# Kernel tuning notes

Measured on AMD Instinct MI355X. Metric: run time of the kernel, lower is better.

## Reference

```python
import jax, jax.numpy as jnp
import numpy as np

B, S, D = 4, 4096, 1024

def setup_inputs() -> dict:
    key = jax.random.key(0)
    ks = jax.random.split(key, 7)
    s = 1.0 / np.sqrt(D)
    return {
        "x": jax.random.normal(ks[0], (B, S, D), dtype=jnp.float32),
        "Wq": jax.random.uniform(ks[1], (D, D), jnp.float32, -s, s),
        "bq": jax.random.uniform(ks[2], (D,), jnp.float32, -s, s),
        "Wk": jax.random.uniform(ks[3], (D, D), jnp.float32, -s, s),
        "bk": jax.random.uniform(ks[4], (D,), jnp.float32, -s, s),
        "Wv": jax.random.uniform(ks[5], (D, D), jnp.float32, -s, s),
        "bv": jax.random.uniform(ks[6], (D,), jnp.float32, -s, s),
    }

def reference(x, Wq, bq, Wk, bk, Wv, bv):
    # q/k/v projections: [B,S,D]
    q = jnp.einsum("bsd,ed->bse", x, Wq) + bq
    k = jnp.einsum("bsd,ed->bse", x, Wk) + bk
    v = jnp.einsum("bsd,ed->bse", x, Wv) + bv
    scale = jnp.asarray(x.shape[-1] ** 0.5, x.dtype)
    scores = jnp.einsum("bqd,bkd->bqk", q, k) / scale  # [B,S,S]
    probs = jax.nn.softmax(scores, axis=-1)
    return jnp.einsum("bqk,bkd->bqd", probs, v)
```

## Files before the change

### kernel.cpp

```cpp
#include <hip/hip_runtime.h>


typedef unsigned short u16;
typedef __attribute__((ext_vector_type(8))) short bf16x8;
typedef __attribute__((ext_vector_type(4))) float f32x4;

__device__ __forceinline__ float bf2f(u16 h) {
    unsigned int x = ((unsigned int)h) << 16;
    float f;
    __builtin_memcpy(&f, &x, 4);
    return f;
}

__device__ __forceinline__ u16 f2bf(float f) {
    unsigned int x;
    __builtin_memcpy(&x, &f, 4);
    unsigned int r = (x + 0x7FFFu + ((x >> 16) & 1u)) >> 16;
    return (u16)r;
}

__device__ __forceinline__ void load16_lds(const u16* g, u16* l) {
    __builtin_amdgcn_global_load_lds(
        (const __attribute__((address_space(1))) void*)g,
        (__attribute__((address_space(3))) void*)l, 16, 0, 0);
}

__global__ __launch_bounds__(256) void cvt_all(
    const float* __restrict__ x, const float* __restrict__ wq,
    const float* __restrict__ wk, const float* __restrict__ wv,
    u16* __restrict__ xo, u16* __restrict__ qo, u16* __restrict__ ko,
    u16* __restrict__ vo, float* __restrict__ L) {
    int i = blockIdx.x * 256 + threadIdx.x;
    if (i >= 4980736) {
        ((float4*)L)[i - 4980736] = (float4){0.f, 0.f, 0.f, 0.f};
        return;
    }
    const float* src;
    u16* dst;
    int idx;
    if (i < 4194304) {
        src = x; dst = xo; idx = i;
    } else {
        int j = i - 4194304;
        int sel = j >> 18;
        idx = j & 262143;
        src = (sel == 0) ? wq : (sel == 1) ? wk : wv;
        dst = (sel == 0) ? qo : (sel == 1) ? ko : vo;
    }
    float4 f = ((const float4*)src)[idx];
    ushort4 o;
    o.x = f2bf(f.x); o.y = f2bf(f.y); o.z = f2bf(f.z); o.w = f2bf(f.w);
    ((ushort4*)dst)[idx] = o;
}

__device__ __forceinline__ void mfma_core(
    const u16* __restrict__ A, const u16* __restrict__ B, int K, int ldA,
    int ldB, size_t rowA0, size_t rowB0, u16* As, u16* Bs, f32x4 acc[4][4]) {
    const int t = threadIdx.x;
    const int lane = t & 63;
    const int wave = t >> 6;
    const int wm = (wave >> 1) * 64;
    const int wn = (wave & 1) * 64;
    const int lm = lane & 15;
    const int qd = lane >> 4;
    const int kx = lm & 7;
    const int rl = lane >> 3;
    const int swz = ((lane & 7) ^ rl) << 3;

#pragma unroll
    for (int i = 0; i < 4; ++i)
#pragma unroll
        for (int j = 0; j < 4; ++j) acc[i][j] = (f32x4){0.f, 0.f, 0.f, 0.f};

    const u16* ga = A + (rowA0 + (size_t)(wave * 32 + rl)) * (size_t)ldA + swz;
    const u16* gb = B + (rowB0 + (size_t)(wave * 32 + rl)) * (size_t)ldB + swz;
    u16* la = As + wave * 2048;
    u16* lb = Bs + wave * 2048;

    for (int kb = 0; kb < K; kb += 64) {
#pragma unroll
        for (int p = 0; p < 4; ++p) {
            load16_lds(ga + (size_t)(p * 8) * ldA + kb, la + p * 512);
            load16_lds(gb + (size_t)(p * 8) * ldB + kb, lb + p * 512);
        }
        __syncthreads();
#pragma unroll
        for (int k0 = 0; k0 < 64; k0 += 32) {
            const int q0 = k0 >> 3;
            const int cofs = (((q0 + qd) ^ kx) << 3);
            bf16x8 a[4], b[4];
#pragma unroll
            for (int i = 0; i < 4; ++i) {
                a[i] = *(const bf16x8*)(As + (wm + i * 16 + lm) * 64 + cofs);
                b[i] = *(const bf16x8*)(Bs + (wn + i * 16 + lm) * 64 + cofs);
            }
#pragma unroll
            for (int i = 0; i < 4; ++i)
#pragma unroll
                for (int j = 0; j < 4; ++j)
                    acc[i][j] = __builtin_amdgcn_mfma_f32_16x16x32_bf16(
                        a[i], b[j], acc[i][j], 0, 0, 0);
        }
        __syncthreads();
    }
}

__global__ __launch_bounds__(256, 4) void proj_qkv(
    const u16* __restrict__ x, const u16* __restrict__ w0,
    const u16* __restrict__ w1, const u16* __restrict__ w2,
    const float* __restrict__ b0, const float* __restrict__ b1,
    const float* __restrict__ b2, u16* __restrict__ Qb, u16* __restrict__ Kb,
    u16* __restrict__ Vt) {
    __shared__ __align__(16) u16 As[128 * 64];
    __shared__ __align__(16) u16 Bs[128 * 64];
    const int z = blockIdx.z;
    const u16* W = (z == 0) ? w0 : (z == 1) ? w1 : w2;
    const float* bias = (z == 0) ? b0 : (z == 1) ? b1 : b2;

    const size_t rowA0 = (size_t)blockIdx.y * 128;
    const size_t rowB0 = (size_t)blockIdx.x * 128;
    f32x4 acc[4][4];
    mfma_core(x, W, 1024, 1024, 1024, rowA0, rowB0, As, Bs, acc);

    const int lane = threadIdx.x & 63;
    const int wave = threadIdx.x >> 6;
    const int wm = (wave >> 1) * 64;
    const int wn = (wave & 1) * 64;
    const int lm = lane & 15;
    const int qd = lane >> 4;

#pragma unroll
    for (int i = 0; i < 4; ++i) {
        const int r0 = (int)rowA0 + wm + i * 16 + qd * 4;
#pragma unroll
        for (int j = 0; j < 4; ++j) {
            const int col = (int)rowB0 + wn + j * 16 + lm;
            const float bv = bias[col];
            if (z < 2) {
                u16* C = z ? Kb : Qb;
#pragma unroll
                for (int r = 0; r < 4; ++r)
                    C[(size_t)(r0 + r) * 1024 + col] = f2bf(acc[i][j][r] + bv);
            } else {
                const int batch = r0 >> 12;
                const int s0 = r0 & 4095;
                ushort4 o;
                o.x = f2bf(acc[i][j][0] + bv);
                o.y = f2bf(acc[i][j][1] + bv);
                o.z = f2bf(acc[i][j][2] + bv);
                o.w = f2bf(acc[i][j][3] + bv);
                *(ushort4*)(Vt + (size_t)batch * 4194304 +
                            (size_t)col * 4096 + s0) = o;
            }
        }
    }
}

__global__ __launch_bounds__(256, 4) void gemm_scores(
    const u16* __restrict__ Qb, const u16* __restrict__ Kb,
    u16* __restrict__ SP, float* __restrict__ L) {
    __shared__ __align__(16) u16 As[128 * 64];
    __shared__ __align__(16) u16 Bs[128 * 64];
    __shared__ float Ls[256];
    const size_t z = blockIdx.z;
    const u16* A = Qb + z * 4194304;
    const u16* B = Kb + z * 4194304;
    u16* C = SP + z * 16777216;

    const size_t rowA0 = (size_t)blockIdx.x * 128;
    const size_t rowB0 = (size_t)blockIdx.y * 128;
    f32x4 acc[4][4];
    mfma_core(A, B, 1024, 1024, 1024, rowA0, rowB0, As, Bs, acc);

    const int lane = threadIdx.x & 63;
    const int wave = threadIdx.x >> 6;
    const int wm = (wave >> 1) * 64;
    const int wn = (wave & 1) * 64;
    const int lm = lane & 15;
    const int qd = lane >> 4;

#pragma unroll
    for (int i = 0; i < 4; ++i) {
        const int rl0 = wm + i * 16 + qd * 4;
        float part[4] = {0.f, 0.f, 0.f, 0.f};
#pragma unroll
        for (int j = 0; j < 4; ++j) {
            const int col = (int)rowB0 + wn + j * 16 + lm;
            u16 o[4];
#pragma unroll
            for (int r = 0; r < 4; ++r) {
                float e = __expf(acc[i][j][r] * 0.03125f);
                o[r] = f2bf(e);
                part[r] += e;
            }
#pragma unroll
            for (int r = 0; r < 4; ++r)
                C[(size_t)(rowA0 + rl0 + r) * 4096 + col] = o[r];
        }
#pragma unroll
        for (int r = 0; r < 4; ++r) {
#pragma unroll
            for (int o = 8; o >= 1; o >>= 1) part[r] += __shfl_xor(part[r], o);
        }
        if (lm == 0) {
#pragma unroll
            for (int r = 0; r < 4; ++r)
                Ls[(rl0 + r) * 2 + (wave & 1)] = part[r];
        }
    }
    __syncthreads();
    const int t = threadIdx.x;
    if (t < 128)
        atomicAdd(L + z * 4096 + rowA0 + t, Ls[t * 2] + Ls[t * 2 + 1]);
}

__global__ __launch_bounds__(256, 4) void gemm_pv(
    const u16* __restrict__ SP, const u16* __restrict__ Vt,
    float* __restrict__ out, const float* __restrict__ L) {
    __shared__ __align__(16) u16 As[128 * 64];
    __shared__ __align__(16) u16 Bs[128 * 64];
    const size_t z = blockIdx.z;
    const u16* A = SP + z * 16777216;
    const u16* B = Vt + z * 4194304;
    float* C = out + z * 4194304;

    const size_t rowA0 = (size_t)blockIdx.x * 128;
    const size_t rowB0 = (size_t)blockIdx.y * 128;
    f32x4 acc[4][4];
    mfma_core(A, B, 4096, 4096, 4096, rowA0, rowB0, As, Bs, acc);

    float* Lsh = (float*)As;
    const int t = threadIdx.x;
    if (t < 128) Lsh[t] = 1.0f / L[z * 4096 + rowA0 + t];
    __syncthreads();

    const int lane = t & 63;
    const int wave = t >> 6;
    const int wm = (wave >> 1) * 64;
    const int wn = (wave & 1) * 64;
    const int lm = lane & 15;
    const int qd = lane >> 4;

#pragma unroll
    for (int i = 0; i < 4; ++i) {
        const int rl0 = wm + i * 16 + qd * 4;
        const int r0 = (int)rowA0 + rl0;
#pragma unroll
        for (int j = 0; j < 4; ++j) {
            const int col = (int)rowB0 + wn + j * 16 + lm;
#pragma unroll
            for (int r = 0; r < 4; ++r)
                C[(size_t)(r0 + r) * 1024 + col] = acc[i][j][r] * Lsh[rl0 + r];
        }
    }
}

template <int MODE>
__global__ __launch_bounds__(256, 3) void gemm_nt(
    const u16* __restrict__ A, const u16* __restrict__ B,
    void* __restrict__ Cv, int K, int ldA, int ldB, int ldC, float scale) {
    __shared__ __align__(16) u16 As[128 * 64];
    __shared__ __align__(16) u16 Bs[128 * 64];
    const size_t rowA0 = (size_t)blockIdx.y * 128;
    const size_t rowB0 = (size_t)blockIdx.x * 128;
    f32x4 acc[4][4];
    mfma_core(A, B, K, ldA, ldB, rowA0, rowB0, As, Bs, acc);

    const int lane = threadIdx.x & 63;
    const int wave = threadIdx.x >> 6;
    const int wm = (wave >> 1) * 64;
    const int wn = (wave & 1) * 64;
    const int lm = lane & 15;
    const int qd = lane >> 4;

#pragma unroll
    for (int i = 0; i < 4; ++i) {
        const int r0 = (int)rowA0 + wm + i * 16 + qd * 4;
#pragma unroll
        for (int j = 0; j < 4; ++j) {
            const int col = (int)rowB0 + wn + j * 16 + lm;
            if (MODE == 2) {
                u16* C = (u16*)Cv;
#pragma unroll
                for (int r = 0; r < 4; ++r)
                    C[(size_t)(r0 + r) * ldC + col] = f2bf(acc[i][j][r] * scale);
            } else {
                float* C = (float*)Cv;
#pragma unroll
                for (int r = 0; r < 4; ++r)
                    C[(size_t)(r0 + r) * ldC + col] = acc[i][j][r];
            }
        }
    }
}

__global__ __launch_bounds__(256) void softmax_inplace(u16* __restrict__ P) {
    u16* p = P + (size_t)blockIdx.x * 4096;
    const int t = threadIdx.x;
    const int lane = t & 63;
    const int wave = t >> 6;
    __shared__ float redmax[4];
    __shared__ float redsum[4];

    uint4 raw0 = *(const uint4*)(p + t * 8);
    uint4 raw1 = *(const uint4*)(p + 2048 + t * 8);
    float v[16];
    {
        const u16* h0 = (const u16*)&raw0;
        const u16* h1 = (const u16*)&raw1;
#pragma unroll
        for (int i = 0; i < 8; ++i) v[i] = bf2f(h0[i]);
#pragma unroll
        for (int i = 0; i < 8; ++i) v[8 + i] = bf2f(h1[i]);
    }
    float m = v[0];
#pragma unroll
    for (int i = 1; i < 16; ++i) m = fmaxf(m, v[i]);
#pragma unroll
    for (int o = 32; o >= 1; o >>= 1) m = fmaxf(m, __shfl_xor(m, o));
    if (lane == 0) redmax[wave] = m;
    __syncthreads();
    m = fmaxf(fmaxf(redmax[0], redmax[1]), fmaxf(redmax[2], redmax[3]));

    float s = 0.f;
#pragma unroll
    for (int i = 0; i < 16; ++i) {
        v[i] = __expf(v[i] - m);
        s += v[i];
    }
#pragma unroll
    for (int o = 32; o >= 1; o >>= 1) s += __shfl_xor(s, o);
    if (lane == 0) redsum[wave] = s;
    __syncthreads();
    s = redsum[0] + redsum[1] + redsum[2] + redsum[3];
    const float inv = 1.0f / s;

    u16 ho[16];
#pragma unroll
    for (int i = 0; i < 16; ++i) ho[i] = f2bf(v[i] * inv);
    *(uint4*)(p + t * 8) = *(const uint4*)&ho[0];
    *(uint4*)(p + 2048 + t * 8) = *(const uint4*)&ho[8];
}

extern "C" void kernel_launch(void* const* d_in, const int* in_sizes, int n_in,
                              void* d_out, int out_size, void* d_ws, size_t ws_size,
                              hipStream_t stream) {
    const float* x  = (const float*)d_in[0];
    const float* Wq = (const float*)d_in[1];
    const float* bq = (const float*)d_in[2];
    const float* Wk = (const float*)d_in[3];
    const float* bk = (const float*)d_in[4];
    const float* Wv = (const float*)d_in[5];
    const float* bv = (const float*)d_in[6];
    float* out = (float*)d_out;

    const bool big = ws_size >= (size_t)234946560;
    char* w = (char*)d_ws;
    u16 *x_bf, *wq_bf, *wk_bf, *wv_bf, *Qb, *Kb, *Vt, *SP;
    float* L = nullptr;
    if (big) {
        SP    = (u16*)(w);
        x_bf  = (u16*)(w);
        wq_bf = (u16*)(w + 33554432);
        wk_bf = (u16*)(w + 35651584);
        wv_bf = (u16*)(w + 37748736);
        Qb    = (u16*)(w + 134217728);
        Kb    = (u16*)(w + 167772160);
        Vt    = (u16*)(w + 201326592);
        L     = (float*)(w + 234881024);
    } else {
        x_bf  = (u16*)(w);
        wq_bf = (u16*)(w + 33554432);
        wk_bf = (u16*)(w + 35651584);
        wv_bf = (u16*)(w + 37748736);
        Qb    = (u16*)(w + 39845888);
        Kb    = (u16*)(w + 73400320);
        Vt    = (u16*)(w + 106954752);
        SP    = (u16*)(w + 140509184);
    }

    cvt_all<<<big ? 19472 : 19456, 256, 0, stream>>>(
        x, Wq, Wk, Wv, x_bf, wq_bf, wk_bf, wv_bf, L);

    proj_qkv<<<dim3(8, 128, 3), 256, 0, stream>>>(
        x_bf, wq_bf, wk_bf, wv_bf, bq, bk, bv, Qb, Kb, Vt);

    if (big) {
        gemm_scores<<<dim3(32, 32, 4), 256, 0, stream>>>(Qb, Kb, SP, L);
        gemm_pv<<<dim3(32, 8, 4), 256, 0, stream>>>(SP, Vt, out, L);
    } else {
        for (int b = 0; b < 4; ++b) {
            const size_t off = (size_t)b * 4194304;
            gemm_nt<2><<<dim3(32, 32, 1), 256, 0, stream>>>(
                Qb + off, Kb + off, SP, 1024, 1024, 1024, 4096, 0.03125f);
            softmax_inplace<<<4096, 256, 0, stream>>>(SP);
            gemm_nt<3><<<dim3(8, 32, 1), 256, 0, stream>>>(
                SP, Vt + off, out + off, 4096, 4096, 4096, 1024, 1.f);
        }
    }
}
```

Measured before the change: 534.0 us.

## Replace scores GEMM with 256x256-tile, 8-wave, double-buffered pipelined kernel

The QK^T scores kernel now uses 256x256 output tiles with 512 threads and 128KB of dynamic LDS. It double-buffers K-slices through direct global-to-LDS loads with swizzled addressing. Explicit waitcnt, barriers and setprio interleave the MFMA phases with the next-stage loads. This is meant to raise data reuse per tile and hide load latency. In exchange it reduces occupancy and adds a large per-thread accumulator footprint, which raises register pressure.

After: 539.2 us. No clear change (+1.0%).

```diff
diff --git a/kernel.cpp b/kernel.cpp
--- a/kernel.cpp
+++ b/kernel.cpp
@@ -156,40 +156,156 @@
     }
 }
 
-__global__ __launch_bounds__(256, 4) void gemm_scores(
+__global__ __launch_bounds__(512, 2) void gemm_scores256(
     const u16* __restrict__ Qb, const u16* __restrict__ Kb,
     u16* __restrict__ SP, float* __restrict__ L) {
-    __shared__ __align__(16) u16 As[128 * 64];
-    __shared__ __align__(16) u16 Bs[128 * 64];
-    __shared__ float Ls[256];
+    extern __shared__ __align__(16) u16 sm[];
     const size_t z = blockIdx.z;
     const u16* A = Qb + z * 4194304;
     const u16* B = Kb + z * 4194304;
     u16* C = SP + z * 16777216;
-
-    const size_t rowA0 = (size_t)blockIdx.x * 128;
-    const size_t rowB0 = (size_t)blockIdx.y * 128;
-    f32x4 acc[4][4];
-    mfma_core(A, B, 1024, 1024, 1024, rowA0, rowB0, As, Bs, acc);
-
-    const int lane = threadIdx.x & 63;
-    const int wave = threadIdx.x >> 6;
-    const int wm = (wave >> 1) * 64;
-    const int wn = (wave & 1) * 64;
-    const int lm = lane & 15;
-    const int qd = lane >> 4;
-
-#pragma unroll
-    for (int i = 0; i < 4; ++i) {
-        const int rl0 = wm + i * 16 + qd * 4;
+    const int rowA0 = blockIdx.x * 256;
+    const int rowB0 = blockIdx.y * 256;
+
+    const int t = threadIdx.x;
+    const int l = t & 63;
+    const int w = t >> 6;
+    const int wr = w >> 2;
+    const int wc = w & 3;
+    const int lm = l & 15;
+    const int qd = l >> 4;
+    const int rsw = (lm >> 1) & 3;
+    const int srow = l >> 2;
+    const int csw = (l & 3) ^ ((l >> 3) & 3);
+    const int roff = (qd ^ rsw) * 8;
+
+    f32x4 acc[8][4];
+#pragma unroll
+    for (int i = 0; i < 8; ++i)
+#pragma unroll
+        for (int j = 0; j < 4; ++j) acc[i][j] = (f32x4){0.f, 0.f, 0.f, 0.f};
+
+    auto STAGE = [&](int M, int s, int ks, int bs) {
+        const u16* G = M ? B : A;
+        const int r0 = M ? rowB0 : rowA0;
+        u16* lb = sm + M * 32768 + bs * 16384 + ks * 8192 + w * 512;
+        const u16* g = G + (size_t)(r0 + w * 16 + srow) * 1024 +
+                       (s * 64 + ks * 32 + csw * 8);
+        load16_lds(g, lb);
+        load16_lds(g + (size_t)128 * 1024, lb + 4096);
+    };
+
+    STAGE(0, 0, 0, 0); STAGE(1, 0, 0, 0);
+    STAGE(0, 0, 1, 0); STAGE(1, 0, 1, 0);
+    STAGE(0, 1, 0, 1); STAGE(1, 1, 0, 1);
+    asm volatile("s_waitcnt vmcnt(8)" ::: "memory");
+    asm volatile("s_barrier" ::: "memory");
+    __builtin_amdgcn_sched_barrier(0);
+
+    const int NS = 16;
+#pragma unroll 2
+    for (int s = 0; s < NS; ++s) {
+        const int cur = s & 1;
+        const u16* As_ = sm + cur * 16384;
+        const u16* Bs_ = sm + 32768 + cur * 16384;
+        bf16x8 a[4], b[4];
+
+#pragma unroll
+        for (int m = 0; m < 4; ++m)
+            a[m] = *(const bf16x8*)(As_ + (wr * 128 + m * 16 + lm) * 32 + roff);
+#pragma unroll
+        for (int n = 0; n < 4; ++n)
+            b[n] = *(const bf16x8*)(Bs_ + (wc * 64 + n * 16 + lm) * 32 + roff);
+        if (s + 1 < NS) STAGE(0, s + 1, 1, (s + 1) & 1);
+        asm volatile("s_barrier" ::: "memory");
+        __builtin_amdgcn_sched_barrier(0);
+        __builtin_amdgcn_s_setprio(1);
+#pragma unroll
+        for (int m = 0; m < 4; ++m)
+#pragma unroll
+            for (int n = 0; n < 4; ++n)
+                acc[m][n] = __builtin_amdgcn_mfma_f32_16x16x32_bf16(
+                    a[m], b[n], acc[m][n], 0, 0, 0);
+        __builtin_amdgcn_s_setprio(0);
+        __builtin_amdgcn_sched_barrier(0);
+        asm volatile("s_barrier" ::: "memory");
+        __builtin_amdgcn_sched_barrier(0);
+
+#pragma unroll
+        for (int m = 0; m < 4; ++m)
+            a[m] = *(const bf16x8*)(As_ + (wr * 128 + 64 + m * 16 + lm) * 32 + roff);
+        if (s + 1 < NS) STAGE(1, s + 1, 1, (s + 1) & 1);
+        if (s < NS - 1) asm volatile("s_waitcnt vmcnt(8)" ::: "memory");
+        else            asm volatile("s_waitcnt vmcnt(0)" ::: "memory");
+        asm volatile("s_barrier" ::: "memory");
+        __builtin_amdgcn_sched_barrier(0);
+        __builtin_amdgcn_s_setprio(1);
+#pragma unroll
+        for (int m = 0; m < 4; ++m)
+#pragma unroll
+            for (int n = 0; n < 4; ++n)
+                acc[4 + m][n] = __builtin_amdgcn_mfma_f32_16x16x32_bf16(
+                    a[m], b[n], acc[4 + m][n], 0, 0, 0);
+        __builtin_amdgcn_s_setprio(0);
+        __builtin_amdgcn_sched_barrier(0);
+        asm volatile("s_barrier" ::: "memory");
+        __builtin_amdgcn_sched_barrier(0);
+
+#pragma unroll
+        for (int m = 0; m < 4; ++m)
+            a[m] = *(const bf16x8*)(As_ + 8192 + (wr * 128 + m * 16 + lm) * 32 + roff);
+#pragma unroll
+        for (int n = 0; n < 4; ++n)
+            b[n] = *(const bf16x8*)(Bs_ + 8192 + (wc * 64 + n * 16 + lm) * 32 + roff);
+        if (s + 2 < NS) STAGE(0, s + 2, 0, s & 1);
+        asm volatile("s_barrier" ::: "memory");
+        __builtin_amdgcn_sched_barrier(0);
+        __builtin_amdgcn_s_setprio(1);
+#pragma unroll
+        for (int m = 0; m < 4; ++m)
+#pragma unroll
+            for (int n = 0; n < 4; ++n)
+                acc[m][n] = __builtin_amdgcn_mfma_f32_16x16x32_bf16(
+                    a[m], b[n], acc[m][n], 0, 0, 0);
+        __builtin_amdgcn_s_setprio(0);
+        __builtin_amdgcn_sched_barrier(0);
+        asm volatile("s_barrier" ::: "memory");
+        __builtin_amdgcn_sched_barrier(0);
+
+#pragma unroll
+        for (int m = 0; m < 4; ++m)
+            a[m] = *(const bf16x8*)(As_ + 8192 + (wr * 128 + 64 + m * 16 + lm) * 32 + roff);
+        if (s + 2 < NS) STAGE(1, s + 2, 0, s & 1);
+        if (s < NS - 2)       asm volatile("s_waitcnt vmcnt(8)" ::: "memory");
+        else if (s == NS - 2) asm volatile("s_waitcnt vmcnt(4)" ::: "memory");
+        else                  asm volatile("s_waitcnt vmcnt(0)" ::: "memory");
+        asm volatile("s_barrier" ::: "memory");
+        __builtin_amdgcn_sched_barrier(0);
+        __builtin_amdgcn_s_setprio(1);
+#pragma unroll
+        for (int m = 0; m < 4; ++m)
+#pragma unroll
+            for (int n = 0; n < 4; ++n)
+                acc[4 + m][n] = __builtin_amdgcn_mfma_f32_16x16x32_bf16(
+                    a[m], b[n], acc[4 + m][n], 0, 0, 0);
+        __builtin_amdgcn_s_setprio(0);
+        __builtin_amdgcn_sched_barrier(0);
+        asm volatile("s_barrier" ::: "memory");
+        __builtin_amdgcn_sched_barrier(0);
+    }
+
+    float* Ls = (float*)sm;
+#pragma unroll
+    for (int i = 0; i < 8; ++i) {
+        const int rl0 = wr * 128 + i * 16 + qd * 4;
         float part[4] = {0.f, 0.f, 0.f, 0.f};
 #pragma unroll
-        for (int j = 0; j < 4; ++j) {
-            const int col = (int)rowB0 + wn + j * 16 + lm;
+        for (int n = 0; n < 4; ++n) {
+            const int col = rowB0 + wc * 64 + n * 16 + lm;
             u16 o[4];
 #pragma unroll
             for (int r = 0; r < 4; ++r) {
-                float e = __expf(acc[i][j][r] * 0.03125f);
+                float e = __expf(acc[i][n][r] * 0.03125f);
                 o[r] = f2bf(e);
                 part[r] += e;
             }
@@ -204,14 +320,13 @@
         }
         if (lm == 0) {
 #pragma unroll
-            for (int r = 0; r < 4; ++r)
-                Ls[(rl0 + r) * 2 + (wave & 1)] = part[r];
+            for (int r = 0; r < 4; ++r) Ls[(rl0 + r) * 4 + wc] = part[r];
         }
     }
     __syncthreads();
-    const int t = threadIdx.x;
-    if (t < 128)
-        atomicAdd(L + z * 4096 + rowA0 + t, Ls[t * 2] + Ls[t * 2 + 1]);
+    if (t < 256)
+        atomicAdd(L + z * 4096 + rowA0 + t,
+                  Ls[t * 4] + Ls[t * 4 + 1] + Ls[t * 4 + 2] + Ls[t * 4 + 3]);
 }
 
 __global__ __launch_bounds__(256, 4) void gemm_pv(
@@ -353,6 +468,13 @@
     const float* Wv = (const float*)d_in[5];
     const float* bv = (const float*)d_in[6];
     float* out = (float*)d_out;
+
+    static bool attr_done = false;
+    if (!attr_done) {
+        hipFuncSetAttribute(reinterpret_cast<const void*>(gemm_scores256),
+                            hipFuncAttributeMaxDynamicSharedMemorySize, 131072);
+        attr_done = true;
+    }
 
     const bool big = ws_size >= (size_t)234946560;
     char* w = (char*)d_ws;
@@ -386,7 +508,7 @@
         x_bf, wq_bf, wk_bf, wv_bf, bq, bk, bv, Qb, Kb, Vt);
 
     if (big) {
-        gemm_scores<<<dim3(32, 32, 4), 256, 0, stream>>>(Qb, Kb, SP, L);
+        gemm_scores256<<<dim3(16, 16, 4), 512, 131072, stream>>>(Qb, Kb, SP, L);
         gemm_pv<<<dim3(32, 8, 4), 256, 0, stream>>>(SP, Vt, out, L);
     } else {
         for (int b = 0; b < 4; ++b) {
```

## Enlarge scores GEMM tile to 256x256 with triple-buffered LDS pipeline

Applied to the files above, without the earlier changes.

Replaces the 128x128 scores kernel with a 256x256-tile, 512-thread kernel that stages Q and K slices via direct global-to-LDS loads into a three-stage ring buffer and uses swizzled LDS addressing. Each wave computes a 128x64 subtile, which raises operand reuse and halves the number of blocks reading Q/K. The softmax-numerator exp and row-sum epilogue is kept, now reducing across four column waves. It needs 96KB of dynamic shared memory and more accumulator registers, which lowers occupancy.

Result: slower. 547.0 us (+2.4%).

```diff
diff --git a/kernel.cpp b/kernel.cpp
--- a/kernel.cpp
+++ b/kernel.cpp
@@ -156,40 +156,89 @@
     }
 }
 
-__global__ __launch_bounds__(256, 4) void gemm_scores(
+__global__ __launch_bounds__(512, 2) void gemm_scores256(
     const u16* __restrict__ Qb, const u16* __restrict__ Kb,
     u16* __restrict__ SP, float* __restrict__ L) {
-    __shared__ __align__(16) u16 As[128 * 64];
-    __shared__ __align__(16) u16 Bs[128 * 64];
-    __shared__ float Ls[256];
+    extern __shared__ __align__(16) u16 sm[];
     const size_t z = blockIdx.z;
-    const u16* A = Qb + z * 4194304;
-    const u16* B = Kb + z * 4194304;
+    const u16* Ag = Qb + z * 4194304;
+    const u16* Bg = Kb + z * 4194304;
     u16* C = SP + z * 16777216;
-
-    const size_t rowA0 = (size_t)blockIdx.x * 128;
-    const size_t rowB0 = (size_t)blockIdx.y * 128;
-    f32x4 acc[4][4];
-    mfma_core(A, B, 1024, 1024, 1024, rowA0, rowB0, As, Bs, acc);
-
-    const int lane = threadIdx.x & 63;
-    const int wave = threadIdx.x >> 6;
-    const int wm = (wave >> 1) * 64;
-    const int wn = (wave & 1) * 64;
-    const int lm = lane & 15;
-    const int qd = lane >> 4;
-
-#pragma unroll
-    for (int i = 0; i < 4; ++i) {
-        const int rl0 = wm + i * 16 + qd * 4;
+    const int rowA0 = blockIdx.x * 256;
+    const int rowB0 = blockIdx.y * 256;
+
+    const int t = threadIdx.x;
+    const int l = t & 63;
+    const int w = t >> 6;
+    const int wr = w >> 2;
+    const int wc = w & 3;
+    const int lm = l & 15;
+    const int qd = l >> 4;
+    const int roff = (qd ^ ((lm >> 1) & 3)) * 8;
+    const int csw = (l & 3) ^ ((l >> 3) & 3);
+
+    f32x4 acc[8][4];
+#pragma unroll
+    for (int i = 0; i < 8; ++i)
+#pragma unroll
+        for (int j = 0; j < 4; ++j) acc[i][j] = (f32x4){0.f, 0.f, 0.f, 0.f};
+
+    auto STAGE = [&](int M, int s, int bs) {
+        const u16* G = M ? Bg : Ag;
+        const int r0 = M ? rowB0 : rowA0;
+        u16* lb = sm + M * 24576 + bs * 8192 + w * 512;
+        const u16* g = G + (size_t)(r0 + w * 16 + (l >> 2)) * 1024 +
+                       (s * 32 + csw * 8);
+        load16_lds(g, lb);
+        load16_lds(g + (size_t)128 * 1024, lb + 4096);
+    };
+
+    STAGE(0, 0, 0); STAGE(1, 0, 0);
+    STAGE(0, 1, 1); STAGE(1, 1, 1);
+    asm volatile("s_waitcnt vmcnt(4)" ::: "memory");
+    asm volatile("s_barrier" ::: "memory");
+
+    const int NS = 32;
+    for (int s = 0; s < NS; ++s) {
+        const int cur = s % 3;
+        if (s + 2 < NS) {
+            const int stg = (s + 2) % 3;
+            STAGE(0, s + 2, stg);
+            STAGE(1, s + 2, stg);
+        }
+        const u16* Ab = sm + cur * 8192;
+        const u16* Bb = sm + 24576 + cur * 8192;
+        bf16x8 a[8], b[4];
+#pragma unroll
+        for (int m = 0; m < 8; ++m)
+            a[m] = *(const bf16x8*)(Ab + (wr * 128 + m * 16 + lm) * 32 + roff);
+#pragma unroll
+        for (int n = 0; n < 4; ++n)
+            b[n] = *(const bf16x8*)(Bb + (wc * 64 + n * 16 + lm) * 32 + roff);
+#pragma unroll
+        for (int m = 0; m < 8; ++m)
+#pragma unroll
+            for (int n = 0; n < 4; ++n)
+                acc[m][n] = __builtin_amdgcn_mfma_f32_16x16x32_bf16(
+                    a[m], b[n], acc[m][n], 0, 0, 0);
+        __builtin_amdgcn_sched_barrier(0);
+        if (s < NS - 2)       asm volatile("s_waitcnt vmcnt(4)" ::: "memory");
+        else if (s == NS - 2) asm volatile("s_waitcnt vmcnt(0)" ::: "memory");
+        asm volatile("s_barrier" ::: "memory");
+    }
+
+    float* Ls = (float*)sm;
+#pragma unroll
+    for (int i = 0; i < 8; ++i) {
+        const int rl0 = wr * 128 + i * 16 + qd * 4;
         float part[4] = {0.f, 0.f, 0.f, 0.f};
 #pragma unroll
-        for (int j = 0; j < 4; ++j) {
-            const int col = (int)rowB0 + wn + j * 16 + lm;
+        for (int n = 0; n < 4; ++n) {
+            const int col = rowB0 + wc * 64 + n * 16 + lm;
             u16 o[4];
 #pragma unroll
             for (int r = 0; r < 4; ++r) {
-                float e = __expf(acc[i][j][r] * 0.03125f);
+                float e = __expf(acc[i][n][r] * 0.03125f);
                 o[r] = f2bf(e);
                 part[r] += e;
             }
@@ -204,14 +253,13 @@
         }
         if (lm == 0) {
 #pragma unroll
-            for (int r = 0; r < 4; ++r)
-                Ls[(rl0 + r) * 2 + (wave & 1)] = part[r];
+            for (int r = 0; r < 4; ++r) Ls[(rl0 + r) * 4 + wc] = part[r];
         }
     }
     __syncthreads();
-    const int t = threadIdx.x;
-    if (t < 128)
-        atomicAdd(L + z * 4096 + rowA0 + t, Ls[t * 2] + Ls[t * 2 + 1]);
+    if (t < 256)
+        atomicAdd(L + z * 4096 + rowA0 + t,
+                  Ls[t * 4] + Ls[t * 4 + 1] + Ls[t * 4 + 2] + Ls[t * 4 + 3]);
 }
 
 __global__ __launch_bounds__(256, 4) void gemm_pv(
@@ -353,6 +401,13 @@
     const float* Wv = (const float*)d_in[5];
     const float* bv = (const float*)d_in[6];
     float* out = (float*)d_out;
+
+    static bool attr_done = false;
+    if (!attr_done) {
+        hipFuncSetAttribute(reinterpret_cast<const void*>(gemm_scores256),
+                            hipFuncAttributeMaxDynamicSharedMemorySize, 98304);
+        attr_done = true;
+    }
 
     const bool big = ws_size >= (size_t)234946560;
     char* w = (char*)d_ws;
@@ -386,7 +441,7 @@
         x_bf, wq_bf, wk_bf, wv_bf, bq, bk, bv, Qb, Kb, Vt);
 
     if (big) {
-        gemm_scores<<<dim3(32, 32, 4), 256, 0, stream>>>(Qb, Kb, SP, L);
+        gemm_scores256<<<dim3(16, 16, 4), 512, 98304, stream>>>(Qb, Kb, SP, L);
         gemm_pv<<<dim3(32, 8, 4), 256, 0, stream>>>(SP, Vt, out, L);
     } else {
         for (int b = 0; b < 4; ++b) {
```

## Rewrite scores GEMM with two waves each computing a 128x64 tile

Applied to the files above, without the earlier changes.

The QK^T scores kernel is restructured to use 128 threads (2 waves) per 128x128 tile instead of 4 waves. Each wave now holds an 8x4 grid of 16x16 MFMA accumulators, which doubles per-wave operand reuse from LDS. The kernel also gets its own inline K loop with swizzled global-to-LDS loads instead of calling the shared mfma_core. The cost is higher register pressure, fewer waves per block and less latency hiding, because the loop is single-buffered with two barriers per K step.

New measurement: 548.4 us. +2.7%, slower.

```diff
diff --git a/kernel.cpp b/kernel.cpp
--- a/kernel.cpp
+++ b/kernel.cpp
@@ -156,7 +156,7 @@
     }
 }
 
-__global__ __launch_bounds__(256, 4) void gemm_scores(
+__global__ __launch_bounds__(128, 2) void gemm_scores(
     const u16* __restrict__ Qb, const u16* __restrict__ Kb,
     u16* __restrict__ SP, float* __restrict__ L) {
     __shared__ __align__(16) u16 As[128 * 64];
@@ -169,27 +169,66 @@
 
     const size_t rowA0 = (size_t)blockIdx.x * 128;
     const size_t rowB0 = (size_t)blockIdx.y * 128;
-    f32x4 acc[4][4];
-    mfma_core(A, B, 1024, 1024, 1024, rowA0, rowB0, As, Bs, acc);
-
-    const int lane = threadIdx.x & 63;
-    const int wave = threadIdx.x >> 6;
-    const int wm = (wave >> 1) * 64;
-    const int wn = (wave & 1) * 64;
+
+    const int t = threadIdx.x;
+    const int lane = t & 63;
+    const int w2 = t >> 6;
     const int lm = lane & 15;
     const int qd = lane >> 4;
-
-#pragma unroll
-    for (int i = 0; i < 4; ++i) {
-        const int rl0 = wm + i * 16 + qd * 4;
+    const int kx = lm & 7;
+    const int rl = lane >> 3;
+    const int swz = ((lane & 7) ^ rl) << 3;
+
+    f32x4 acc[8][4];
+#pragma unroll
+    for (int m = 0; m < 8; ++m)
+#pragma unroll
+        for (int n = 0; n < 4; ++n) acc[m][n] = (f32x4){0.f, 0.f, 0.f, 0.f};
+
+    const u16* ga = A + (rowA0 + (size_t)(w2 * 64 + rl)) * 1024 + swz;
+    const u16* gb = B + (rowB0 + (size_t)(w2 * 64 + rl)) * 1024 + swz;
+    u16* la = As + w2 * 4096;
+    u16* lb = Bs + w2 * 4096;
+
+    for (int kb = 0; kb < 1024; kb += 64) {
+#pragma unroll
+        for (int p = 0; p < 8; ++p) {
+            load16_lds(ga + (size_t)(p * 8) * 1024 + kb, la + p * 512);
+            load16_lds(gb + (size_t)(p * 8) * 1024 + kb, lb + p * 512);
+        }
+        __syncthreads();
+#pragma unroll
+        for (int k0 = 0; k0 < 64; k0 += 32) {
+            const int q0 = k0 >> 3;
+            const int cofs = (((q0 + qd) ^ kx) << 3);
+            bf16x8 a[8], b[4];
+#pragma unroll
+            for (int m = 0; m < 8; ++m)
+                a[m] = *(const bf16x8*)(As + (m * 16 + lm) * 64 + cofs);
+#pragma unroll
+            for (int n = 0; n < 4; ++n)
+                b[n] = *(const bf16x8*)(Bs + (w2 * 64 + n * 16 + lm) * 64 + cofs);
+#pragma unroll
+            for (int m = 0; m < 8; ++m)
+#pragma unroll
+                for (int n = 0; n < 4; ++n)
+                    acc[m][n] = __builtin_amdgcn_mfma_f32_16x16x32_bf16(
+                        a[m], b[n], acc[m][n], 0, 0, 0);
+        }
+        __syncthreads();
+    }
+
+#pragma unroll
+    for (int m = 0; m < 8; ++m) {
+        const int rl0 = m * 16 + qd * 4;
         float part[4] = {0.f, 0.f, 0.f, 0.f};
 #pragma unroll
-        for (int j = 0; j < 4; ++j) {
-            const int col = (int)rowB0 + wn + j * 16 + lm;
+        for (int n = 0; n < 4; ++n) {
+            const int col = (int)rowB0 + w2 * 64 + n * 16 + lm;
             u16 o[4];
 #pragma unroll
             for (int r = 0; r < 4; ++r) {
-                float e = __expf(acc[i][j][r] * 0.03125f);
+                float e = __expf(acc[m][n][r] * 0.03125f);
                 o[r] = f2bf(e);
                 part[r] += e;
             }
@@ -204,12 +243,10 @@
         }
         if (lm == 0) {
 #pragma unroll
-            for (int r = 0; r < 4; ++r)
-                Ls[(rl0 + r) * 2 + (wave & 1)] = part[r];
+            for (int r = 0; r < 4; ++r) Ls[(rl0 + r) * 2 + w2] = part[r];
         }
     }
     __syncthreads();
-    const int t = threadIdx.x;
     if (t < 128)
         atomicAdd(L + z * 4096 + rowA0 + t, Ls[t * 2] + Ls[t * 2 + 1]);
 }
@@ -386,7 +423,7 @@
         x_bf, wq_bf, wk_bf, wv_bf, bq, bk, bv, Qb, Kb, Vt);
 
     if (big) {
-        gemm_scores<<<dim3(32, 32, 4), 256, 0, stream>>>(Qb, Kb, SP, L);
+        gemm_scores<<<dim3(32, 32, 4), 128, 0, stream>>>(Qb, Kb, SP, L);
         gemm_pv<<<dim3(32, 8, 4), 256, 0, stream>>>(SP, Vt, out, L);
     } else {
         for (int b = 0; b < 4; ++b) {
```
